# Kernel optimization log

Measured on AMD Instinct MI355X. Metric: run time of the kernel, lower is better.

The kernel has to match this reference:

```python
import jax, jax.numpy as jnp
import numpy as np

B, T, C = 4, 2048, 1024
H = 16
D = C // H  # head_dim = 64


def setup_inputs() -> dict:
    key = jax.random.key(0)
    ks = jax.random.split(key, 9)
    s = 1.0 / np.sqrt(C)
    return {
        "x": jax.random.normal(ks[0], (B, T, C), dtype=jnp.float32),
        "Wk": jax.random.uniform(ks[1], (C, C), jnp.float32, -s, s),
        "bk": jax.random.uniform(ks[2], (C,), jnp.float32, -s, s),
        "Wq": jax.random.uniform(ks[3], (C, C), jnp.float32, -s, s),
        "bq": jax.random.uniform(ks[4], (C,), jnp.float32, -s, s),
        "Wv": jax.random.uniform(ks[5], (C, C), jnp.float32, -s, s),
        "bv": jax.random.uniform(ks[6], (C,), jnp.float32, -s, s),
        "Wp": jax.random.uniform(ks[7], (C, C), jnp.float32, -s, s),
        "bp": jax.random.uniform(ks[8], (C,), jnp.float32, -s, s),
    }


def reference(x, Wk, bk, Wq, bq, Wv, bv, Wp, bp):
    # projections -> (B, H, T, D)
    def split_heads(y):
        return y.reshape(B, T, H, D).transpose(0, 2, 1, 3)

    k = split_heads(x @ Wk.T + bk)
    q = split_heads(x @ Wq.T + bq)
    v = split_heads(x @ Wv.T + bv)

    att = jnp.einsum("bhtd,bhsd->bhts", q, k) / np.sqrt(D).astype(np.float32)
    causal = jnp.tril(jnp.ones((T, T), dtype=bool))
    att = jnp.where(causal, att, -jnp.inf)
    att = jax.nn.softmax(att, axis=-1)

    y = jnp.einsum("bhts,bhsd->bhtd", att, v)  # (B,H,T,D)
    y = y.transpose(0, 2, 1, 3).reshape(B, T, C)
    return y @ Wp.T + bp
```

## Files before the change

### kernel.cpp

```cpp
#include <hip/hip_runtime.h>
#include <hip/hip_bf16.h>

typedef unsigned short u16;
typedef unsigned int u32;
typedef short short8 __attribute__((ext_vector_type(8)));
typedef short short4v __attribute__((ext_vector_type(4)));
typedef float f32x4 __attribute__((ext_vector_type(4)));
typedef unsigned int u32x4 __attribute__((ext_vector_type(4)));

#define MFMA16(a, b, c) __builtin_amdgcn_mfma_f32_16x16x32_bf16((a), (b), (c), 0, 0, 0)

constexpr int kB = 4, kT = 2048, kC = 1024, kH = 16, kD = 64;
constexpr int kBT = kB * kT;
constexpr long kQKV = (long)kB * kH * kT * kD;
constexpr float kSC = 0.125f * 1.4426950408889634f;

__device__ inline u16 f2bf(float f) {
    __hip_bfloat16 h = __float2bfloat16(f);
    return *reinterpret_cast<u16*>(&h);
}
__device__ inline u32 pkbf_trunc(float lo, float hi) {
    return __builtin_amdgcn_perm(__builtin_bit_cast(u32, hi),
                                 __builtin_bit_cast(u32, lo), 0x07060302u);
}
__device__ inline u32 pkbf_rne(float lo, float hi) {
    return ((u32)f2bf(hi) << 16) | (u32)f2bf(lo);
}

__device__ inline void cp16(const u16* g, u16* l) {
    __builtin_amdgcn_global_load_lds(
        (const __attribute__((address_space(1))) unsigned int*)g,
        (__attribute__((address_space(3))) unsigned int*)l, 16, 0, 0);
}

__global__ __launch_bounds__(256) void cast_kernel(
    const float* __restrict__ x,  const float* __restrict__ Wk,
    const float* __restrict__ Wq, const float* __restrict__ Wv,
    const float* __restrict__ Wp,
    u16* __restrict__ xb, u16* __restrict__ wkb, u16* __restrict__ wqb,
    u16* __restrict__ wvb, u16* __restrict__ wpb)
{
    const long id = (long)blockIdx.x * 256 + threadIdx.x;
    const float* src;
    u16* dst;
    long off;
    if (id < 2097152) {
        src = x; dst = xb; off = id;
    } else {
        const long w = (id - 2097152) >> 18;
        off = (id - 2097152) & 262143;
        src = (w == 0) ? Wk : (w == 1) ? Wq : (w == 2) ? Wv : Wp;
        dst = (w == 0) ? wkb : (w == 1) ? wqb : (w == 2) ? wvb : wpb;
    }
    f32x4 v = *(const f32x4*)&src[off * 4];
    short4v s = {(short)f2bf(v[0]), (short)f2bf(v[1]),
                 (short)f2bf(v[2]), (short)f2bf(v[3])};
    *(short4v*)&dst[off * 4] = s;
}


__global__ __launch_bounds__(256, 2) void qkv_gemm_bf16(
    const u16* __restrict__ xb, const u16* __restrict__ wall,
    const float* __restrict__ bk, const float* __restrict__ bq,
    const float* __restrict__ bv,
    u16* __restrict__ kw, u16* __restrict__ qw, u16* __restrict__ vw)
{
    __shared__ __align__(16) u16 A2[2][128 * 64];
    __shared__ __align__(16) u16 B2[2][128 * 64];

    const int tid = threadIdx.x;
    const int lane = tid & 63;
    const int wid = tid >> 6;
    const int l15 = lane & 15;
    const int quad = lane >> 4;
    const int wr = wid & 1;
    const int wc = wid >> 1;
    const int m0 = blockIdx.x * 128;
    const int n0c = blockIdx.y * 128;

    f32x4 zero = {0.f, 0.f, 0.f, 0.f};
    f32x4 acc[4][4];
#pragma unroll
    for (int i = 0; i < 4; ++i)
#pragma unroll
        for (int j = 0; j < 4; ++j) acc[i][j] = zero;

    const u16* aMaS[2]; const u16* aMbS[2];
    const u16* bNaS[2]; const u16* bNbS[2];
    int aMaD[2], aMbD[2], bNaD[2], bNbD[2];
#pragma unroll
    for (int q = 0; q < 2; ++q) {
        const int slot = q * 256 + tid;
        const int v = slot >> 3, ch = slot & 7;
        const int ra = ((v >> 5) << 6) + (v & 31);
        const int rb = ra + 32;
        aMaS[q] = xb + (long)(m0 + ra) * kC + ((ch ^ (ra & 7)) * 8);
        aMbS[q] = xb + (long)(m0 + rb) * kC + ((ch ^ (rb & 7)) * 8);
        aMaD[q] = ra * 64 + ch * 8;
        aMbD[q] = rb * 64 + ch * 8;
        bNaS[q] = wall + (long)(n0c + ra) * kC + ((ch ^ (ra & 7)) * 8);
        bNbS[q] = wall + (long)(n0c + rb) * kC + ((ch ^ (rb & 7)) * 8);
        bNaD[q] = ra * 64 + ch * 8;
        bNbD[q] = rb * 64 + ch * 8;
    }

    int aOff[4][2], bOff[4][2];
#pragma unroll
    for (int i = 0; i < 4; ++i) {
        const int row = wr * 64 + i * 16 + l15;
#pragma unroll
        for (int k2 = 0; k2 < 2; ++k2)
            aOff[i][k2] = row * 64 + (((k2 * 4 + quad) ^ (row & 7)) * 8);
    }
#pragma unroll
    for (int j = 0; j < 4; ++j) {
        const int row = wc * 64 + j * 16 + l15;
#pragma unroll
        for (int k2 = 0; k2 < 2; ++k2)
            bOff[j][k2] = row * 64 + (((k2 * 4 + quad) ^ (row & 7)) * 8);
    }

    cp16(bNaS[0], &B2[0][bNaD[0]]);
    cp16(bNaS[1], &B2[0][bNaD[1]]);
    cp16(aMaS[0], &A2[0][aMaD[0]]);
    cp16(aMaS[1], &A2[0][aMaD[1]]);
    cp16(aMbS[0], &A2[0][aMbD[0]]);
    cp16(aMbS[1], &A2[0][aMbD[1]]);
    cp16(bNbS[0], &B2[0][bNbD[0]]);
    cp16(bNbS[1], &B2[0][bNbD[1]]);

#pragma unroll 2
    for (int t = 0; t < 16; ++t) {
        const int c = t & 1;
        const u16* Ab = A2[c];
        const u16* Bb = B2[c];
        u16* An = A2[c ^ 1];
        u16* Bn = B2[c ^ 1];
        const long ko = (long)(t + 1) * 64;
        const bool pf = (t < 15);

        short8 amL[2][2], amH[2][2], bnL[2][2], bnH[2][2];

        asm volatile("s_waitcnt vmcnt(2)" ::: "memory");
        __builtin_amdgcn_s_barrier();
        __builtin_amdgcn_sched_barrier(0);
#pragma unroll
        for (int i = 0; i < 2; ++i)
#pragma unroll
            for (int k2 = 0; k2 < 2; ++k2)
                amL[i][k2] = *(const short8*)&Ab[aOff[i][k2]];
#pragma unroll
        for (int j = 0; j < 2; ++j)
#pragma unroll
            for (int k2 = 0; k2 < 2; ++k2)
                bnL[j][k2] = *(const short8*)&Bb[bOff[j][k2]];
        if (pf) {
            cp16(bNaS[0] + ko, &Bn[bNaD[0]]);
            cp16(bNaS[1] + ko, &Bn[bNaD[1]]);
        }
        asm volatile("s_waitcnt lgkmcnt(0)" ::: "memory");
        __builtin_amdgcn_sched_barrier(0);
        __builtin_amdgcn_s_setprio(1);
#pragma unroll
        for (int i = 0; i < 2; ++i)
#pragma unroll
            for (int j = 0; j < 2; ++j) {
                acc[i][j] = MFMA16(amL[i][0], bnL[j][0], acc[i][j]);
                acc[i][j] = MFMA16(amL[i][1], bnL[j][1], acc[i][j]);
            }
        __builtin_amdgcn_s_setprio(0);

#pragma unroll
        for (int i = 0; i < 2; ++i)
#pragma unroll
            for (int k2 = 0; k2 < 2; ++k2)
                amH[i][k2] = *(const short8*)&Ab[aOff[2 + i][k2]];
        if (pf) {
            cp16(aMaS[0] + ko, &An[aMaD[0]]);
            cp16(aMaS[1] + ko, &An[aMaD[1]]);
            cp16(aMbS[0] + ko, &An[aMbD[0]]);
            cp16(aMbS[1] + ko, &An[aMbD[1]]);
        }
        asm volatile("s_waitcnt lgkmcnt(0)" ::: "memory");
        __builtin_amdgcn_sched_barrier(0);
        __builtin_amdgcn_s_setprio(1);
#pragma unroll
        for (int i = 0; i < 2; ++i)
#pragma unroll
            for (int j = 0; j < 2; ++j) {
                acc[2 + i][j] = MFMA16(amH[i][0], bnL[j][0], acc[2 + i][j]);
                acc[2 + i][j] = MFMA16(amH[i][1], bnL[j][1], acc[2 + i][j]);
            }
        __builtin_amdgcn_s_setprio(0);

        if (pf) {
            asm volatile("s_waitcnt vmcnt(6)" ::: "memory");
        } else {
            asm volatile("s_waitcnt vmcnt(0)" ::: "memory");
        }
        __builtin_amdgcn_s_barrier();
        __builtin_amdgcn_sched_barrier(0);
#pragma unroll
        for (int j = 0; j < 2; ++j)
#pragma unroll
            for (int k2 = 0; k2 < 2; ++k2)
                bnH[j][k2] = *(const short8*)&Bb[bOff[2 + j][k2]];
        if (pf) {
            cp16(bNbS[0] + ko, &Bn[bNbD[0]]);
            cp16(bNbS[1] + ko, &Bn[bNbD[1]]);
        }
        asm volatile("s_waitcnt lgkmcnt(0)" ::: "memory");
        __builtin_amdgcn_sched_barrier(0);
        __builtin_amdgcn_s_setprio(1);
#pragma unroll
        for (int i = 0; i < 2; ++i)
#pragma unroll
            for (int j = 0; j < 2; ++j) {
                acc[i][2 + j] = MFMA16(amL[i][0], bnH[j][0], acc[i][2 + j]);
                acc[i][2 + j] = MFMA16(amL[i][1], bnH[j][1], acc[i][2 + j]);
            }
        __builtin_amdgcn_s_setprio(0);

        __builtin_amdgcn_s_setprio(1);
#pragma unroll
        for (int i = 0; i < 2; ++i)
#pragma unroll
            for (int j = 0; j < 2; ++j) {
                acc[2 + i][2 + j] = MFMA16(amH[i][0], bnH[j][0], acc[2 + i][2 + j]);
                acc[2 + i][2 + j] = MFMA16(amH[i][1], bnH[j][1], acc[2 + i][2 + j]);
            }
        __builtin_amdgcn_s_setprio(0);
    }

    const int z = (n0c >> 10);
    const float scale = (z == 1) ? kSC : 1.0f;
    const float* bias = (z == 0) ? bk : (z == 1) ? bq : bv;
#pragma unroll
    for (int j = 0; j < 4; ++j) {
        const int n = n0c + wc * 64 + j * 16 + l15;
        const int np = n & 1023;
        const float bias_f = bias[np];
        const int h = np >> 6, d = np & 63;
#pragma unroll
        for (int i = 0; i < 4; ++i) {
#pragma unroll
            for (int r = 0; r < 4; ++r) {
                const int m = m0 + wr * 64 + i * 16 + quad * 4 + r;
                const int b = m >> 11, tt = m & 2047;
                const float v = (acc[i][j][r] + bias_f) * scale;
                const int bh = b * kH + h;
                if (z == 2) {
                    vw[((long)bh * kD + d) * kT + tt] = f2bf(v);
                } else {
                    u16* dst = (z == 0) ? kw : qw;
                    dst[((long)bh * kT + tt) * kD + d] = f2bf(v);
                }
            }
        }
    }
}

__global__ __launch_bounds__(256) void qkv_gemm_kernel(
    const float* __restrict__ x,
    const float* __restrict__ Wk, const float* __restrict__ bk,
    const float* __restrict__ Wq, const float* __restrict__ bq,
    const float* __restrict__ Wv, const float* __restrict__ bv,
    u16* __restrict__ kw, u16* __restrict__ qw, u16* __restrict__ vw)
{
    __shared__ u16 As[128 * 32];
    __shared__ u16 Bs[128 * 32];
    const int tid = threadIdx.x;
    const int lane = tid & 63;
    const int wid = tid >> 6;
    const int l15 = lane & 15;
    const int quad = lane >> 4;
    const int m0 = blockIdx.x * 128;
    const int n0 = blockIdx.y * 128;
    const int z = blockIdx.z;

    const float* W = (z == 0) ? Wk : (z == 1) ? Wq : Wv;
    const float* bias = (z == 0) ? bk : (z == 1) ? bq : bv;

    f32x4 zero = {0.f, 0.f, 0.f, 0.f};
    f32x4 acc[4][4];
#pragma unroll
    for (int i = 0; i < 4; ++i)
#pragma unroll
        for (int j = 0; j < 4; ++j) acc[i][j] = zero;

    const int wm = (wid & 1) * 64;
    const int wn = (wid >> 1) * 64;
    const int row4 = tid >> 3;
    const int col4 = (tid & 7) * 4;

    for (int k0 = 0; k0 < kC; k0 += 32) {
#pragma unroll
        for (int p = 0; p < 4; ++p) {
            const int r = p * 32 + row4;
            f32x4 xa = *(const f32x4*)&x[(long)(m0 + r) * kC + k0 + col4];
            f32x4 wa = *(const f32x4*)&W[(long)(n0 + r) * kC + k0 + col4];
            short4v xs = {(short)f2bf(xa[0]), (short)f2bf(xa[1]),
                          (short)f2bf(xa[2]), (short)f2bf(xa[3])};
            short4v wsv = {(short)f2bf(wa[0]), (short)f2bf(wa[1]),
                           (short)f2bf(wa[2]), (short)f2bf(wa[3])};
            *(short4v*)&As[r * 32 + col4] = xs;
            *(short4v*)&Bs[r * 32 + col4] = wsv;
        }
        __syncthreads();
        short8 af[4], bfr[4];
#pragma unroll
        for (int mt = 0; mt < 4; ++mt)
            af[mt] = *(const short8*)&As[(wm + mt * 16 + l15) * 32 + quad * 8];
#pragma unroll
        for (int nt = 0; nt < 4; ++nt)
            bfr[nt] = *(const short8*)&Bs[(wn + nt * 16 + l15) * 32 + quad * 8];
#pragma unroll
        for (int mt = 0; mt < 4; ++mt)
#pragma unroll
            for (int nt = 0; nt < 4; ++nt)
                acc[mt][nt] = MFMA16(af[mt], bfr[nt], acc[mt][nt]);
        __syncthreads();
    }

    const float scale = (z == 1) ? kSC : 1.0f;
#pragma unroll
    for (int nt = 0; nt < 4; ++nt) {
        const int n = n0 + wn + nt * 16 + l15;
        const float bias_f = bias[n];
        const int h = n >> 6, d = n & 63;
#pragma unroll
        for (int mt = 0; mt < 4; ++mt) {
#pragma unroll
            for (int r = 0; r < 4; ++r) {
                const int m = m0 + wm + mt * 16 + quad * 4 + r;
                const int b = m >> 11, t = m & 2047;
                const float v = (acc[mt][nt][r] + bias_f) * scale;
                const int bh = b * kH + h;
                if (z == 2) {
                    vw[((long)bh * kD + d) * kT + t] = f2bf(v);
                } else {
                    u16* dst = (z == 0) ? kw : qw;
                    dst[((long)bh * kT + t) * kD + d] = f2bf(v);
                }
            }
        }
    }
}

__global__ __launch_bounds__(256, 4) void attn_kernel(
    const u16* qw, const u16* kw, const u16* vw, u16* ow)
{
    __shared__ u16 Ks[2][64 * 64];
    __shared__ u16 VT[2][64 * 64];

    const int tid = threadIdx.x;
    const int lane = tid & 63;
    const int wid = tid >> 6;
    const int l15 = lane & 15;
    const int quad = lane >> 4;
    const int id = blockIdx.x;
    const int bh = id & 63;
    constexpr int pperm[16] = {15, 14, 13, 12, 0, 1, 2, 3,
                               11, 10, 9, 8, 4, 5, 6, 7};
    const int p = pperm[id >> 6];
    const int p2 = 2 * p;
    const int n_st = p2 + 2;
    const int tw = p * 128 + wid * 32;

    const float NEG = -1.0e30f;
    f32x4 zero = {0.f, 0.f, 0.f, 0.f};
    const short8 onesf = {(short)0x3F80, (short)0x3F80, (short)0x3F80, (short)0x3F80,
                          (short)0x3F80, (short)0x3F80, (short)0x3F80, (short)0x3F80};

    const int rl7 = l15 & 7;

    const u16* kbase = kw + (long)bh * kT * kD;
    const u16* vbase = vw + (long)bh * kD * kT;

    const u16* kp[2];
    const u16* vp[2];
    int sdst[2];
#pragma unroll
    for (int q = 0; q < 2; ++q) {
        const int slot = q * 256 + tid;
        const int row = slot >> 3;
        const int c = slot & 7;
        const int off = (c ^ (row & 7)) * 8;
        kp[q] = kbase + (long)row * kD + off;
        vp[q] = vbase + (long)row * kT + off;
        sdst[q] = slot * 8;
    }

    auto stage = [&](int buf, int st) {
        u16* kd = Ks[buf];
        u16* vd = VT[buf];
#pragma unroll
        for (int q = 0; q < 2; ++q) {
            cp16(kp[q] + (long)st * (64 * kD), kd + sdst[q]);
            cp16(vp[q] + st * 64,              vd + sdst[q]);
        }
    };

    short8 qf[2][2];
#pragma unroll
    for (int g = 0; g < 2; ++g) {
        const u16* qp = qw + ((long)bh * kT + tw + g * 16 + l15) * kD;
        qf[g][0] = *(const short8*)&qp[quad * 8];
        qf[g][1] = *(const short8*)&qp[32 + quad * 8];
    }

    stage(0, 0);
    stage(1, 1);
    __syncthreads();

    f32x4 oacc[4][2];
#pragma unroll
    for (int mo = 0; mo < 4; ++mo)
#pragma unroll
        for (int g = 0; g < 2; ++g) oacc[mo][g] = zero;
    f32x4 lsum[2] = {zero, zero};

    for (int st = 0; st < n_st; ++st) {
        const int cur = st & 1;
        const u16* K_ = Ks[cur];
        const u16* V_ = VT[cur];

        f32x4 sacc[4][2];
        __builtin_amdgcn_s_setprio(1);
#pragma unroll
        for (int ms = 0; ms < 4; ++ms) {
            const int row = ms * 16 + l15;
            short8 kf0 = *(const short8*)&K_[row * 64 + ((quad ^ rl7) * 8)];
            short8 kf1 = *(const short8*)&K_[row * 64 + (((4 + quad) ^ rl7) * 8)];
#pragma unroll
            for (int g = 0; g < 2; ++g) {
                sacc[ms][g] = MFMA16(kf0, qf[g][0], zero);
                sacc[ms][g] = MFMA16(kf1, qf[g][1], sacc[ms][g]);
            }
        }
        __builtin_amdgcn_s_setprio(0);

        const int dg = st - p2;
        if (dg >= 0) {
#pragma unroll
            for (int g = 0; g < 2; ++g) {
                const int off = wid * 32 + g * 16 + l15 - dg * 64;
#pragma unroll
                for (int ms = 0; ms < 4; ++ms)
#pragma unroll
                    for (int r = 0; r < 4; ++r)
                        if (ms * 16 + quad * 4 + r > off) sacc[ms][g][r] = NEG;
            }
        }

        short8 pfr[2][2];
#pragma unroll
        for (int g = 0; g < 2; ++g) {
#pragma unroll
            for (int k2 = 0; k2 < 2; ++k2) {
                const int msA = k2 * 2, msB = k2 * 2 + 1;
                const float a0 = exp2f(sacc[msA][g][0]);
                const float a1 = exp2f(sacc[msA][g][1]);
                const float a2 = exp2f(sacc[msA][g][2]);
                const float a3 = exp2f(sacc[msA][g][3]);
                const float b0 = exp2f(sacc[msB][g][0]);
                const float b1 = exp2f(sacc[msB][g][1]);
                const float b2 = exp2f(sacc[msB][g][2]);
                const float b3 = exp2f(sacc[msB][g][3]);
                const u32 LA = pkbf_trunc(a0, a1), HA = pkbf_trunc(a2, a3);
                const u32 LB = pkbf_trunc(b0, b1), HB = pkbf_trunc(b2, b3);
                auto pL = __builtin_amdgcn_permlane32_swap(LA, LB, false, false);
                auto pH = __builtin_amdgcn_permlane32_swap(HA, HB, false, false);
                auto rL = __builtin_amdgcn_permlane16_swap(pL[0], pL[1], false, false);
                auto rH = __builtin_amdgcn_permlane16_swap(pH[0], pH[1], false, false);
                u32x4 w;
                w[0] = rL[0]; w[1] = rH[0]; w[2] = rL[1]; w[3] = rH[1];
                pfr[g][k2] = __builtin_bit_cast(short8, w);
            }
        }

#pragma unroll
        for (int g = 0; g < 2; ++g) {
            lsum[g] = MFMA16(onesf, pfr[g][0], lsum[g]);
            lsum[g] = MFMA16(onesf, pfr[g][1], lsum[g]);
        }

        __builtin_amdgcn_s_setprio(1);
#pragma unroll
        for (int mo = 0; mo < 4; ++mo) {
            const int row = mo * 16 + l15;
            short8 vf0 = *(const short8*)&V_[row * 64 + ((quad ^ rl7) * 8)];
            short8 vf1 = *(const short8*)&V_[row * 64 + (((4 + quad) ^ rl7) * 8)];
#pragma unroll
            for (int g = 0; g < 2; ++g) {
                oacc[mo][g] = MFMA16(vf0, pfr[g][0], oacc[mo][g]);
                oacc[mo][g] = MFMA16(vf1, pfr[g][1], oacc[mo][g]);
            }
        }
        __builtin_amdgcn_s_setprio(0);

        if (st + 1 < n_st) {
            __syncthreads();
            if (st + 2 < n_st) stage(cur, st + 2);
        }
    }

#pragma unroll
    for (int g = 0; g < 2; ++g) {
        const float inv = 1.0f / lsum[g][0];
        const int t = tw + g * 16 + l15;
        u16* op = ow + ((long)bh * kT + t) * kD;
#pragma unroll
        for (int mo = 0; mo < 4; ++mo) {
            uint2 ov;
            ov.x = pkbf_rne(oacc[mo][g][0] * inv, oacc[mo][g][1] * inv);
            ov.y = pkbf_rne(oacc[mo][g][2] * inv, oacc[mo][g][3] * inv);
            *(uint2*)&op[mo * 16 + quad * 4] = ov;
        }
    }
}

__global__ __launch_bounds__(256, 2) void out_gemm_bf16(
    const u16* __restrict__ ob, const u16* __restrict__ wpb,
    const float* __restrict__ bp, float* __restrict__ out)
{
    __shared__ __align__(16) u16 A2[2][128 * 64];
    __shared__ __align__(16) u16 B2[2][128 * 64];

    const int tid = threadIdx.x;
    const int lane = tid & 63;
    const int wid = tid >> 6;
    const int l15 = lane & 15;
    const int quad = lane >> 4;
    const int wr = wid & 1;
    const int wc = wid >> 1;
    const int m0 = blockIdx.x * 128;
    const int n0 = blockIdx.y * 128;

    f32x4 zero = {0.f, 0.f, 0.f, 0.f};
    f32x4 acc[4][4];
#pragma unroll
    for (int i = 0; i < 4; ++i)
#pragma unroll
        for (int j = 0; j < 4; ++j) acc[i][j] = zero;

    const u16* aMaS[2]; const u16* aMbS[2];
    const u16* bNaS[2]; const u16* bNbS[2];
    int aMaD[2], aMbD[2], bNaD[2], bNbD[2];
#pragma unroll
    for (int q = 0; q < 2; ++q) {
        const int slot = q * 256 + tid;
        const int v = slot >> 3, ch = slot & 7;
        const int ra = ((v >> 5) << 6) + (v & 31);
        const int rb = ra + 32;
        const int mA = m0 + ra, mB = m0 + rb;
        aMaS[q] = ob + (((long)(mA >> 11) * kH) * kT + (mA & 2047)) * kD
                  + ((ch ^ (ra & 7)) * 8);
        aMbS[q] = ob + (((long)(mB >> 11) * kH) * kT + (mB & 2047)) * kD
                  + ((ch ^ (rb & 7)) * 8);
        aMaD[q] = ra * 64 + ch * 8;
        aMbD[q] = rb * 64 + ch * 8;
        bNaS[q] = wpb + (long)(n0 + ra) * kC + ((ch ^ (ra & 7)) * 8);
        bNbS[q] = wpb + (long)(n0 + rb) * kC + ((ch ^ (rb & 7)) * 8);
        bNaD[q] = ra * 64 + ch * 8;
        bNbD[q] = rb * 64 + ch * 8;
    }

    int aOff[4][2], bOff[4][2];
#pragma unroll
    for (int i = 0; i < 4; ++i) {
        const int row = wr * 64 + i * 16 + l15;
#pragma unroll
        for (int k2 = 0; k2 < 2; ++k2)
            aOff[i][k2] = row * 64 + (((k2 * 4 + quad) ^ (row & 7)) * 8);
    }
#pragma unroll
    for (int j = 0; j < 4; ++j) {
        const int row = wc * 64 + j * 16 + l15;
#pragma unroll
        for (int k2 = 0; k2 < 2; ++k2)
            bOff[j][k2] = row * 64 + (((k2 * 4 + quad) ^ (row & 7)) * 8);
    }

    cp16(bNaS[0], &B2[0][bNaD[0]]);
    cp16(bNaS[1], &B2[0][bNaD[1]]);
    cp16(aMaS[0], &A2[0][aMaD[0]]);
    cp16(aMaS[1], &A2[0][aMaD[1]]);
    cp16(aMbS[0], &A2[0][aMbD[0]]);
    cp16(aMbS[1], &A2[0][aMbD[1]]);
    cp16(bNbS[0], &B2[0][bNbD[0]]);
    cp16(bNbS[1], &B2[0][bNbD[1]]);

#pragma unroll 2
    for (int t = 0; t < 16; ++t) {
        const int c = t & 1;
        const u16* Ab = A2[c];
        const u16* Bb = B2[c];
        u16* An = A2[c ^ 1];
        u16* Bn = B2[c ^ 1];
        const long koA = (long)(t + 1) * kT * kD;
        const long koB = (long)(t + 1) * 64;
        const bool pf = (t < 15);

        short8 amL[2][2], amH[2][2], bnL[2][2], bnH[2][2];

        asm volatile("s_waitcnt vmcnt(2)" ::: "memory");
        __builtin_amdgcn_s_barrier();
        __builtin_amdgcn_sched_barrier(0);
#pragma unroll
        for (int i = 0; i < 2; ++i)
#pragma unroll
            for (int k2 = 0; k2 < 2; ++k2)
                amL[i][k2] = *(const short8*)&Ab[aOff[i][k2]];
#pragma unroll
        for (int j = 0; j < 2; ++j)
#pragma unroll
            for (int k2 = 0; k2 < 2; ++k2)
                bnL[j][k2] = *(const short8*)&Bb[bOff[j][k2]];
        if (pf) {
            cp16(bNaS[0] + koB, &Bn[bNaD[0]]);
            cp16(bNaS[1] + koB, &Bn[bNaD[1]]);
        }
        asm volatile("s_waitcnt lgkmcnt(0)" ::: "memory");
        __builtin_amdgcn_sched_barrier(0);
        __builtin_amdgcn_s_setprio(1);
#pragma unroll
        for (int i = 0; i < 2; ++i)
#pragma unroll
            for (int j = 0; j < 2; ++j) {
                acc[i][j] = MFMA16(amL[i][0], bnL[j][0], acc[i][j]);
                acc[i][j] = MFMA16(amL[i][1], bnL[j][1], acc[i][j]);
            }
        __builtin_amdgcn_s_setprio(0);

#pragma unroll
        for (int i = 0; i < 2; ++i)
#pragma unroll
            for (int k2 = 0; k2 < 2; ++k2)
                amH[i][k2] = *(const short8*)&Ab[aOff[2 + i][k2]];
        if (pf) {
            cp16(aMaS[0] + koA, &An[aMaD[0]]);
            cp16(aMaS[1] + koA, &An[aMaD[1]]);
            cp16(aMbS[0] + koA, &An[aMbD[0]]);
            cp16(aMbS[1] + koA, &An[aMbD[1]]);
        }
        asm volatile("s_waitcnt lgkmcnt(0)" ::: "memory");
        __builtin_amdgcn_sched_barrier(0);
        __builtin_amdgcn_s_setprio(1);
#pragma unroll
        for (int i = 0; i < 2; ++i)
#pragma unroll
            for (int j = 0; j < 2; ++j) {
                acc[2 + i][j] = MFMA16(amH[i][0], bnL[j][0], acc[2 + i][j]);
                acc[2 + i][j] = MFMA16(amH[i][1], bnL[j][1], acc[2 + i][j]);
            }
        __builtin_amdgcn_s_setprio(0);

        if (pf) {
            asm volatile("s_waitcnt vmcnt(6)" ::: "memory");
        } else {
            asm volatile("s_waitcnt vmcnt(0)" ::: "memory");
        }
        __builtin_amdgcn_s_barrier();
        __builtin_amdgcn_sched_barrier(0);
#pragma unroll
        for (int j = 0; j < 2; ++j)
#pragma unroll
            for (int k2 = 0; k2 < 2; ++k2)
                bnH[j][k2] = *(const short8*)&Bb[bOff[2 + j][k2]];
        if (pf) {
            cp16(bNbS[0] + koB, &Bn[bNbD[0]]);
            cp16(bNbS[1] + koB, &Bn[bNbD[1]]);
        }
        asm volatile("s_waitcnt lgkmcnt(0)" ::: "memory");
        __builtin_amdgcn_sched_barrier(0);
        __builtin_amdgcn_s_setprio(1);
#pragma unroll
        for (int i = 0; i < 2; ++i)
#pragma unroll
            for (int j = 0; j < 2; ++j) {
                acc[i][2 + j] = MFMA16(amL[i][0], bnH[j][0], acc[i][2 + j]);
                acc[i][2 + j] = MFMA16(amL[i][1], bnH[j][1], acc[i][2 + j]);
            }
        __builtin_amdgcn_s_setprio(0);

        __builtin_amdgcn_s_setprio(1);
#pragma unroll
        for (int i = 0; i < 2; ++i)
#pragma unroll
            for (int j = 0; j < 2; ++j) {
                acc[2 + i][2 + j] = MFMA16(amH[i][0], bnH[j][0], acc[2 + i][2 + j]);
                acc[2 + i][2 + j] = MFMA16(amH[i][1], bnH[j][1], acc[2 + i][2 + j]);
            }
        __builtin_amdgcn_s_setprio(0);
    }

#pragma unroll
    for (int j = 0; j < 4; ++j) {
        const int n = n0 + wc * 64 + j * 16 + l15;
        const float bias_f = bp[n];
#pragma unroll
        for (int i = 0; i < 4; ++i) {
#pragma unroll
            for (int r = 0; r < 4; ++r) {
                const int m = m0 + wr * 64 + i * 16 + quad * 4 + r;
                out[(long)m * kC + n] = acc[i][j][r] + bias_f;
            }
        }
    }
}

__global__ __launch_bounds__(256) void out_gemm_kernel(
    const u16* __restrict__ ow, const float* __restrict__ Wp,
    const float* __restrict__ bp, float* __restrict__ out)
{
    __shared__ u16 As[128 * 32];
    __shared__ u16 Bs[128 * 32];
    const int tid = threadIdx.x;
    const int lane = tid & 63;
    const int wid = tid >> 6;
    const int l15 = lane & 15;
    const int quad = lane >> 4;
    const int m0 = blockIdx.x * 128;
    const int n0 = blockIdx.y * 128;

    f32x4 zero = {0.f, 0.f, 0.f, 0.f};
    f32x4 acc[4][4];
#pragma unroll
    for (int i = 0; i < 4; ++i)
#pragma unroll
        for (int j = 0; j < 4; ++j) acc[i][j] = zero;

    const int wm = (wid & 1) * 64;
    const int wn = (wid >> 1) * 64;

    const int r0 = tid >> 2;
    const int kkA = (tid & 3) * 8;
    const int r1 = r0 + 64;
    const int row4 = tid >> 3;
    const int col4 = (tid & 7) * 4;

    for (int k0 = 0; k0 < kC; k0 += 32) {
        {
            const int m = m0 + r0, b = m >> 11, t = m & 2047;
            const int kk = k0 + kkA, h = kk >> 6, d = kk & 63;
            *(short8*)&As[r0 * 32 + kkA] =
                *(const short8*)&ow[(((long)b * kH + h) * kT + t) * kD + d];
        }
        {
            const int m = m0 + r1, b = m >> 11, t = m & 2047;
            const int kk = k0 + kkA, h = kk >> 6, d = kk & 63;
            *(short8*)&As[r1 * 32 + kkA] =
                *(const short8*)&ow[(((long)b * kH + h) * kT + t) * kD + d];
        }
#pragma unroll
        for (int p = 0; p < 4; ++p) {
            const int r = p * 32 + row4;
            f32x4 wa = *(const f32x4*)&Wp[(long)(n0 + r) * kC + k0 + col4];
            short4v wsv = {(short)f2bf(wa[0]), (short)f2bf(wa[1]),
                           (short)f2bf(wa[2]), (short)f2bf(wa[3])};
            *(short4v*)&Bs[r * 32 + col4] = wsv;
        }
        __syncthreads();
        short8 af[4], bfr[4];
#pragma unroll
        for (int mt = 0; mt < 4; ++mt)
            af[mt] = *(const short8*)&As[(wm + mt * 16 + l15) * 32 + quad * 8];
#pragma unroll
        for (int nt = 0; nt < 4; ++nt)
            bfr[nt] = *(const short8*)&Bs[(wn + nt * 16 + l15) * 32 + quad * 8];
#pragma unroll
        for (int mt = 0; mt < 4; ++mt)
#pragma unroll
            for (int nt = 0; nt < 4; ++nt)
                acc[mt][nt] = MFMA16(af[mt], bfr[nt], acc[mt][nt]);
        __syncthreads();
    }

#pragma unroll
    for (int nt = 0; nt < 4; ++nt) {
        const int n = n0 + wn + nt * 16 + l15;
        const float bias_f = bp[n];
#pragma unroll
        for (int mt = 0; mt < 4; ++mt) {
#pragma unroll
            for (int r = 0; r < 4; ++r) {
                const int m = m0 + wm + mt * 16 + quad * 4 + r;
                out[(long)m * kC + n] = acc[mt][nt][r] + bias_f;
            }
        }
    }
}

extern "C" void kernel_launch(void* const* d_in, const int* in_sizes, int n_in,
                              void* d_out, int out_size, void* d_ws, size_t ws_size,
                              hipStream_t stream) {
    const float* x  = (const float*)d_in[0];
    const float* Wk = (const float*)d_in[1];
    const float* bk = (const float*)d_in[2];
    const float* Wq = (const float*)d_in[3];
    const float* bq = (const float*)d_in[4];
    const float* Wv = (const float*)d_in[5];
    const float* bv = (const float*)d_in[6];
    const float* Wp = (const float*)d_in[7];
    const float* bp = (const float*)d_in[8];
    float* out = (float*)d_out;

    u16* ws = (u16*)d_ws;
    const size_t kNeed = 72ull * 1024 * 1024;

    if (ws_size >= kNeed) {
        u16* k_ws = ws;
        u16* q_ws = ws + kQKV;
        u16* v_ws = ws + 2 * kQKV;
        u16* xb   = ws + 3 * kQKV;
        u16* o_ws = xb;
        u16* wkb  = ws + 4 * kQKV;
        u16* wqb  = wkb + (long)kC * kC;
        u16* wvb  = wqb + (long)kC * kC;
        u16* wpb  = wvb + (long)kC * kC;

        cast_kernel<<<12288, 256, 0, stream>>>(x, Wk, Wq, Wv, Wp,
                                               xb, wkb, wqb, wvb, wpb);
        qkv_gemm_bf16<<<dim3(kBT / 128, 24), 256, 0, stream>>>(
            xb, wkb, bk, bq, bv, k_ws, q_ws, v_ws);
        attn_kernel<<<1024, 256, 0, stream>>>(q_ws, k_ws, v_ws, o_ws);
        out_gemm_bf16<<<dim3(kBT / 128, kC / 128), 256, 0, stream>>>(
            o_ws, wpb, bp, out);
    } else {
        u16* k_ws = ws;
        u16* q_ws = ws + kQKV;
        u16* v_ws = ws + 2 * kQKV;
        u16* o_ws = q_ws;

        qkv_gemm_kernel<<<dim3(kBT / 128, kC / 128, 3), 256, 0, stream>>>(
            x, Wk, bk, Wq, bq, Wv, bv, k_ws, q_ws, v_ws);
        attn_kernel<<<1024, 256, 0, stream>>>(q_ws, k_ws, v_ws, o_ws);
        out_gemm_kernel<<<dim3(kBT / 128, kC / 128), 256, 0, stream>>>(
            o_ws, Wp, bp, out);
    }
}
```

Measured before the change: 260.5 us.

## Use 512-thread blocks with simplified double-buffered pipeline in bf16 GEMMs

Both bf16 GEMM kernels (QKV and output projection) move from 4 waves per 128x128 tile to 8 waves, with each wave computing a 64x32 sub-tile. The hand-interleaved split-phase pipeline, with its explicit vmcnt waits and staggered prefetches, is replaced by a plain double buffer: stage two k-tiles up front, then __syncthreads and prefetch k-tile t+2 each iteration. The aim is more waves to hide latency and simpler code. In exchange, launch bounds of (512,4) put heavy pressure on registers, which can cause spills. LDS of 64KB per block limits how many blocks actually co-reside, and much of the fine-grained overlap of loads with MFMA work is lost.

```diff
diff --git a/kernel.cpp b/kernel.cpp
--- a/kernel.cpp
+++ b/kernel.cpp
@@ -59,7 +59,7 @@
 }
 
 
-__global__ __launch_bounds__(256, 2) void qkv_gemm_bf16(
+__global__ __launch_bounds__(512, 4) void qkv_gemm_bf16(
     const u16* __restrict__ xb, const u16* __restrict__ wall,
     const float* __restrict__ bk, const float* __restrict__ bq,
     const float* __restrict__ bv,
@@ -79,32 +79,33 @@
     const int n0c = blockIdx.y * 128;
 
     f32x4 zero = {0.f, 0.f, 0.f, 0.f};
-    f32x4 acc[4][4];
+    f32x4 acc[4][2];
 #pragma unroll
     for (int i = 0; i < 4; ++i)
 #pragma unroll
-        for (int j = 0; j < 4; ++j) acc[i][j] = zero;
-
-    const u16* aMaS[2]; const u16* aMbS[2];
-    const u16* bNaS[2]; const u16* bNbS[2];
-    int aMaD[2], aMbD[2], bNaD[2], bNbD[2];
+        for (int j = 0; j < 2; ++j) acc[i][j] = zero;
+
+    const u16* aS[2]; const u16* bS[2];
+    int sD[2];
 #pragma unroll
     for (int q = 0; q < 2; ++q) {
-        const int slot = q * 256 + tid;
-        const int v = slot >> 3, ch = slot & 7;
-        const int ra = ((v >> 5) << 6) + (v & 31);
-        const int rb = ra + 32;
-        aMaS[q] = xb + (long)(m0 + ra) * kC + ((ch ^ (ra & 7)) * 8);
-        aMbS[q] = xb + (long)(m0 + rb) * kC + ((ch ^ (rb & 7)) * 8);
-        aMaD[q] = ra * 64 + ch * 8;
-        aMbD[q] = rb * 64 + ch * 8;
-        bNaS[q] = wall + (long)(n0c + ra) * kC + ((ch ^ (ra & 7)) * 8);
-        bNbS[q] = wall + (long)(n0c + rb) * kC + ((ch ^ (rb & 7)) * 8);
-        bNaD[q] = ra * 64 + ch * 8;
-        bNbD[q] = rb * 64 + ch * 8;
-    }
-
-    int aOff[4][2], bOff[4][2];
+        const int slot = q * 512 + tid;
+        const int row = slot >> 3, ch = slot & 7;
+        aS[q] = xb + (long)(m0 + row) * kC + ((ch ^ (row & 7)) * 8);
+        bS[q] = wall + (long)(n0c + row) * kC + ((ch ^ (row & 7)) * 8);
+        sD[q] = row * 64 + ch * 8;
+    }
+
+    auto stage = [&](int buf, int t) {
+        const long ko = (long)t * 64;
+#pragma unroll
+        for (int q = 0; q < 2; ++q) {
+            cp16(aS[q] + ko, &A2[buf][sD[q]]);
+            cp16(bS[q] + ko, &B2[buf][sD[q]]);
+        }
+    };
+
+    int aOff[4][2], bOff[2][2];
 #pragma unroll
     for (int i = 0; i < 4; ++i) {
         const int row = wr * 64 + i * 16 + l15;
@@ -113,131 +114,56 @@
             aOff[i][k2] = row * 64 + (((k2 * 4 + quad) ^ (row & 7)) * 8);
     }
 #pragma unroll
-    for (int j = 0; j < 4; ++j) {
-        const int row = wc * 64 + j * 16 + l15;
+    for (int j = 0; j < 2; ++j) {
+        const int row = wc * 32 + j * 16 + l15;
 #pragma unroll
         for (int k2 = 0; k2 < 2; ++k2)
             bOff[j][k2] = row * 64 + (((k2 * 4 + quad) ^ (row & 7)) * 8);
     }
 
-    cp16(bNaS[0], &B2[0][bNaD[0]]);
-    cp16(bNaS[1], &B2[0][bNaD[1]]);
-    cp16(aMaS[0], &A2[0][aMaD[0]]);
-    cp16(aMaS[1], &A2[0][aMaD[1]]);
-    cp16(aMbS[0], &A2[0][aMbD[0]]);
-    cp16(aMbS[1], &A2[0][aMbD[1]]);
-    cp16(bNbS[0], &B2[0][bNbD[0]]);
-    cp16(bNbS[1], &B2[0][bNbD[1]]);
-
-#pragma unroll 2
+    stage(0, 0);
+    stage(1, 1);
+    __syncthreads();
+
     for (int t = 0; t < 16; ++t) {
         const int c = t & 1;
         const u16* Ab = A2[c];
         const u16* Bb = B2[c];
-        u16* An = A2[c ^ 1];
-        u16* Bn = B2[c ^ 1];
-        const long ko = (long)(t + 1) * 64;
-        const bool pf = (t < 15);
-
-        short8 amL[2][2], amH[2][2], bnL[2][2], bnH[2][2];
-
-        asm volatile("s_waitcnt vmcnt(2)" ::: "memory");
-        __builtin_amdgcn_s_barrier();
-        __builtin_amdgcn_sched_barrier(0);
-#pragma unroll
-        for (int i = 0; i < 2; ++i)
+
+        short8 am[4][2], bn[2][2];
+#pragma unroll
+        for (int i = 0; i < 4; ++i)
 #pragma unroll
             for (int k2 = 0; k2 < 2; ++k2)
-                amL[i][k2] = *(const short8*)&Ab[aOff[i][k2]];
+                am[i][k2] = *(const short8*)&Ab[aOff[i][k2]];
 #pragma unroll
         for (int j = 0; j < 2; ++j)
 #pragma unroll
             for (int k2 = 0; k2 < 2; ++k2)
-                bnL[j][k2] = *(const short8*)&Bb[bOff[j][k2]];
-        if (pf) {
-            cp16(bNaS[0] + ko, &Bn[bNaD[0]]);
-            cp16(bNaS[1] + ko, &Bn[bNaD[1]]);
-        }
-        asm volatile("s_waitcnt lgkmcnt(0)" ::: "memory");
-        __builtin_amdgcn_sched_barrier(0);
+                bn[j][k2] = *(const short8*)&Bb[bOff[j][k2]];
+
         __builtin_amdgcn_s_setprio(1);
 #pragma unroll
-        for (int i = 0; i < 2; ++i)
+        for (int i = 0; i < 4; ++i)
 #pragma unroll
             for (int j = 0; j < 2; ++j) {
-                acc[i][j] = MFMA16(amL[i][0], bnL[j][0], acc[i][j]);
-                acc[i][j] = MFMA16(amL[i][1], bnL[j][1], acc[i][j]);
+                acc[i][j] = MFMA16(am[i][0], bn[j][0], acc[i][j]);
+                acc[i][j] = MFMA16(am[i][1], bn[j][1], acc[i][j]);
             }
         __builtin_amdgcn_s_setprio(0);
 
-#pragma unroll
-        for (int i = 0; i < 2; ++i)
-#pragma unroll
-            for (int k2 = 0; k2 < 2; ++k2)
-                amH[i][k2] = *(const short8*)&Ab[aOff[2 + i][k2]];
-        if (pf) {
-            cp16(aMaS[0] + ko, &An[aMaD[0]]);
-            cp16(aMaS[1] + ko, &An[aMaD[1]]);
-            cp16(aMbS[0] + ko, &An[aMbD[0]]);
-            cp16(aMbS[1] + ko, &An[aMbD[1]]);
-        }
-        asm volatile("s_waitcnt lgkmcnt(0)" ::: "memory");
-        __builtin_amdgcn_sched_barrier(0);
-        __builtin_amdgcn_s_setprio(1);
-#pragma unroll
-        for (int i = 0; i < 2; ++i)
-#pragma unroll
-            for (int j = 0; j < 2; ++j) {
-                acc[2 + i][j] = MFMA16(amH[i][0], bnL[j][0], acc[2 + i][j]);
-                acc[2 + i][j] = MFMA16(amH[i][1], bnL[j][1], acc[2 + i][j]);
-            }
-        __builtin_amdgcn_s_setprio(0);
-
-        if (pf) {
-            asm volatile("s_waitcnt vmcnt(6)" ::: "memory");
-        } else {
-            asm volatile("s_waitcnt vmcnt(0)" ::: "memory");
-        }
-        __builtin_amdgcn_s_barrier();
-        __builtin_amdgcn_sched_barrier(0);
-#pragma unroll
-        for (int j = 0; j < 2; ++j)
-#pragma unroll
-            for (int k2 = 0; k2 < 2; ++k2)
-                bnH[j][k2] = *(const short8*)&Bb[bOff[2 + j][k2]];
-        if (pf) {
-            cp16(bNbS[0] + ko, &Bn[bNbD[0]]);
-            cp16(bNbS[1] + ko, &Bn[bNbD[1]]);
-        }
-        asm volatile("s_waitcnt lgkmcnt(0)" ::: "memory");
-        __builtin_amdgcn_sched_barrier(0);
-        __builtin_amdgcn_s_setprio(1);
-#pragma unroll
-        for (int i = 0; i < 2; ++i)
-#pragma unroll
-            for (int j = 0; j < 2; ++j) {
-                acc[i][2 + j] = MFMA16(amL[i][0], bnH[j][0], acc[i][2 + j]);
-                acc[i][2 + j] = MFMA16(amL[i][1], bnH[j][1], acc[i][2 + j]);
-            }
-        __builtin_amdgcn_s_setprio(0);
-
-        __builtin_amdgcn_s_setprio(1);
-#pragma unroll
-        for (int i = 0; i < 2; ++i)
-#pragma unroll
-            for (int j = 0; j < 2; ++j) {
-                acc[2 + i][2 + j] = MFMA16(amH[i][0], bnH[j][0], acc[2 + i][2 + j]);
-                acc[2 + i][2 + j] = MFMA16(amH[i][1], bnH[j][1], acc[2 + i][2 + j]);
-            }
-        __builtin_amdgcn_s_setprio(0);
+        if (t + 1 < 16) {
+            __syncthreads();
+            if (t + 2 < 16) stage(c, t + 2);
+        }
     }
 
     const int z = (n0c >> 10);
     const float scale = (z == 1) ? kSC : 1.0f;
     const float* bias = (z == 0) ? bk : (z == 1) ? bq : bv;
 #pragma unroll
-    for (int j = 0; j < 4; ++j) {
-        const int n = n0c + wc * 64 + j * 16 + l15;
+    for (int j = 0; j < 2; ++j) {
+        const int n = n0c + wc * 32 + j * 16 + l15;
         const int np = n & 1023;
         const float bias_f = bias[np];
         const int h = np >> 6, d = np & 63;
@@ -520,7 +446,7 @@
     }
 }
 
-__global__ __launch_bounds__(256, 2) void out_gemm_bf16(
+__global__ __launch_bounds__(512, 4) void out_gemm_bf16(
     const u16* __restrict__ ob, const u16* __restrict__ wpb,
     const float* __restrict__ bp, float* __restrict__ out)
 {
@@ -538,35 +464,35 @@
     const int n0 = blockIdx.y * 128;
 
     f32x4 zero = {0.f, 0.f, 0.f, 0.f};
-    f32x4 acc[4][4];
+    f32x4 acc[4][2];
 #pragma unroll
     for (int i = 0; i < 4; ++i)
 #pragma unroll
-        for (int j = 0; j < 4; ++j) acc[i][j] = zero;
-
-    const u16* aMaS[2]; const u16* aMbS[2];
-    const u16* bNaS[2]; const u16* bNbS[2];
-    int aMaD[2], aMbD[2], bNaD[2], bNbD[2];
+        for (int j = 0; j < 2; ++j) acc[i][j] = zero;
+
+    const u16* aS[2]; const u16* bS[2];
+    int sD[2];
 #pragma unroll
     for (int q = 0; q < 2; ++q) {
-        const int slot = q * 256 + tid;
-        const int v = slot >> 3, ch = slot & 7;
-        const int ra = ((v >> 5) << 6) + (v & 31);
-        const int rb = ra + 32;
-        const int mA = m0 + ra, mB = m0 + rb;
-        aMaS[q] = ob + (((long)(mA >> 11) * kH) * kT + (mA & 2047)) * kD
-                  + ((ch ^ (ra & 7)) * 8);
-        aMbS[q] = ob + (((long)(mB >> 11) * kH) * kT + (mB & 2047)) * kD
-                  + ((ch ^ (rb & 7)) * 8);
-        aMaD[q] = ra * 64 + ch * 8;
-        aMbD[q] = rb * 64 + ch * 8;
-        bNaS[q] = wpb + (long)(n0 + ra) * kC + ((ch ^ (ra & 7)) * 8);
-        bNbS[q] = wpb + (long)(n0 + rb) * kC + ((ch ^ (rb & 7)) * 8);
-        bNaD[q] = ra * 64 + ch * 8;
-        bNbD[q] = rb * 64 + ch * 8;
-    }
-
-    int aOff[4][2], bOff[4][2];
+        const int slot = q * 512 + tid;
+        const int row = slot >> 3, ch = slot & 7;
+        const int m = m0 + row, b = m >> 11, trow = m & 2047;
+        aS[q] = ob + (((long)b * kH) * kT + trow) * kD + ((ch ^ (row & 7)) * 8);
+        bS[q] = wpb + (long)(n0 + row) * kC + ((ch ^ (row & 7)) * 8);
+        sD[q] = row * 64 + ch * 8;
+    }
+
+    auto stage = [&](int buf, int t) {
+        const long koA = (long)t * kT * kD;
+        const long koB = (long)t * 64;
+#pragma unroll
+        for (int q = 0; q < 2; ++q) {
+            cp16(aS[q] + koA, &A2[buf][sD[q]]);
+            cp16(bS[q] + koB, &B2[buf][sD[q]]);
+        }
+    };
+
+    int aOff[4][2], bOff[2][2];
 #pragma unroll
     for (int i = 0; i < 4; ++i) {
         const int row = wr * 64 + i * 16 + l15;
@@ -575,129 +501,53 @@
             aOff[i][k2] = row * 64 + (((k2 * 4 + quad) ^ (row & 7)) * 8);
     }
 #pragma unroll
-    for (int j = 0; j < 4; ++j) {
-        const int row = wc * 64 + j * 16 + l15;
+    for (int j = 0; j < 2; ++j) {
+        const int row = wc * 32 + j * 16 + l15;
 #pragma unroll
         for (int k2 = 0; k2 < 2; ++k2)
             bOff[j][k2] = row * 64 + (((k2 * 4 + quad) ^ (row & 7)) * 8);
     }
 
-    cp16(bNaS[0], &B2[0][bNaD[0]]);
-    cp16(bNaS[1], &B2[0][bNaD[1]]);
-    cp16(aMaS[0], &A2[0][aMaD[0]]);
-    cp16(aMaS[1], &A2[0][aMaD[1]]);
-    cp16(aMbS[0], &A2[0][aMbD[0]]);
-    cp16(aMbS[1], &A2[0][aMbD[1]]);
-    cp16(bNbS[0], &B2[0][bNbD[0]]);
-    cp16(bNbS[1], &B2[0][bNbD[1]]);
-
-#pragma unroll 2
+    stage(0, 0);
+    stage(1, 1);
+    __syncthreads();
+
     for (int t = 0; t < 16; ++t) {
         const int c = t & 1;
         const u16* Ab = A2[c];
         const u16* Bb = B2[c];
-        u16* An = A2[c ^ 1];
-        u16* Bn = B2[c ^ 1];
-        const long koA = (long)(t + 1) * kT * kD;
-        const long koB = (long)(t + 1) * 64;
-        const bool pf = (t < 15);
-
-        short8 amL[2][2], amH[2][2], bnL[2][2], bnH[2][2];
-
-        asm volatile("s_waitcnt vmcnt(2)" ::: "memory");
-        __builtin_amdgcn_s_barrier();
-        __builtin_amdgcn_sched_barrier(0);
-#pragma unroll
-        for (int i = 0; i < 2; ++i)
+
+        short8 am[4][2], bn[2][2];
+#pragma unroll
+        for (int i = 0; i < 4; ++i)
 #pragma unroll
             for (int k2 = 0; k2 < 2; ++k2)
-                amL[i][k2] = *(const short8*)&Ab[aOff[i][k2]];
+                am[i][k2] = *(const short8*)&Ab[aOff[i][k2]];
 #pragma unroll
         for (int j = 0; j < 2; ++j)
 #pragma unroll
             for (int k2 = 0; k2 < 2; ++k2)
-                bnL[j][k2] = *(const short8*)&Bb[bOff[j][k2]];
-        if (pf) {
-            cp16(bNaS[0] + koB, &Bn[bNaD[0]]);
-            cp16(bNaS[1] + koB, &Bn[bNaD[1]]);
-        }
-        asm volatile("s_waitcnt lgkmcnt(0)" ::: "memory");
-        __builtin_amdgcn_sched_barrier(0);
+                bn[j][k2] = *(const short8*)&Bb[bOff[j][k2]];
+
         __builtin_amdgcn_s_setprio(1);
 #pragma unroll
-        for (int i = 0; i < 2; ++i)
+        for (int i = 0; i < 4; ++i)
 #pragma unroll
             for (int j = 0; j < 2; ++j) {
-                acc[i][j] = MFMA16(amL[i][0], bnL[j][0], acc[i][j]);
-                acc[i][j] = MFMA16(amL[i][1], bnL[j][1], acc[i][j]);
+                acc[i][j] = MFMA16(am[i][0], bn[j][0], acc[i][j]);
+                acc[i][j] = MFMA16(am[i][1], bn[j][1], acc[i][j]);
             }
         __builtin_amdgcn_s_setprio(0);
 
-#pragma unroll
-        for (int i = 0; i < 2; ++i)
-#pragma unroll
-            for (int k2 = 0; k2 < 2; ++k2)
-                amH[i][k2] = *(const short8*)&Ab[aOff[2 + i][k2]];
-        if (pf) {
-            cp16(aMaS[0] + koA, &An[aMaD[0]]);
-            cp16(aMaS[1] + koA, &An[aMaD[1]]);
-            cp16(aMbS[0] + koA, &An[aMbD[0]]);
-            cp16(aMbS[1] + koA, &An[aMbD[1]]);
-        }
-        asm volatile("s_waitcnt lgkmcnt(0)" ::: "memory");
-        __builtin_amdgcn_sched_barrier(0);
-        __builtin_amdgcn_s_setprio(1);
-#pragma unroll
-        for (int i = 0; i < 2; ++i)
-#pragma unroll
-            for (int j = 0; j < 2; ++j) {
-                acc[2 + i][j] = MFMA16(amH[i][0], bnL[j][0], acc[2 + i][j]);
-                acc[2 + i][j] = MFMA16(amH[i][1], bnL[j][1], acc[2 + i][j]);
-            }
-        __builtin_amdgcn_s_setprio(0);
-
-        if (pf) {
-            asm volatile("s_waitcnt vmcnt(6)" ::: "memory");
-        } else {
-            asm volatile("s_waitcnt vmcnt(0)" ::: "memory");
-        }
-        __builtin_amdgcn_s_barrier();
-        __builtin_amdgcn_sched_barrier(0);
-#pragma unroll
-        for (int j = 0; j < 2; ++j)
-#pragma unroll
-            for (int k2 = 0; k2 < 2; ++k2)
-                bnH[j][k2] = *(const short8*)&Bb[bOff[2 + j][k2]];
-        if (pf) {
-            cp16(bNbS[0] + koB, &Bn[bNbD[0]]);
-            cp16(bNbS[1] + koB, &Bn[bNbD[1]]);
-        }
-        asm volatile("s_waitcnt lgkmcnt(0)" ::: "memory");
-        __builtin_amdgcn_sched_barrier(0);
-        __builtin_amdgcn_s_setprio(1);
-#pragma unroll
-        for (int i = 0; i < 2; ++i)
-#pragma unroll
-            for (int j = 0; j < 2; ++j) {
-                acc[i][2 + j] = MFMA16(amL[i][0], bnH[j][0], acc[i][2 + j]);
-                acc[i][2 + j] = MFMA16(amL[i][1], bnH[j][1], acc[i][2 + j]);
-            }
-        __builtin_amdgcn_s_setprio(0);
-
-        __builtin_amdgcn_s_setprio(1);
-#pragma unroll
-        for (int i = 0; i < 2; ++i)
-#pragma unroll
-            for (int j = 0; j < 2; ++j) {
-                acc[2 + i][2 + j] = MFMA16(amH[i][0], bnH[j][0], acc[2 + i][2 + j]);
-                acc[2 + i][2 + j] = MFMA16(amH[i][1], bnH[j][1], acc[2 + i][2 + j]);
-            }
-        __builtin_amdgcn_s_setprio(0);
-    }
-
-#pragma unroll
-    for (int j = 0; j < 4; ++j) {
-        const int n = n0 + wc * 64 + j * 16 + l15;
+        if (t + 1 < 16) {
+            __syncthreads();
+            if (t + 2 < 16) stage(c, t + 2);
+        }
+    }
+
+#pragma unroll
+    for (int j = 0; j < 2; ++j) {
+        const int n = n0 + wc * 32 + j * 16 + l15;
         const float bias_f = bp[n];
 #pragma unroll
         for (int i = 0; i < 4; ++i) {
@@ -822,10 +672,10 @@
 
         cast_kernel<<<12288, 256, 0, stream>>>(x, Wk, Wq, Wv, Wp,
                                                xb, wkb, wqb, wvb, wpb);
-        qkv_gemm_bf16<<<dim3(kBT / 128, 24), 256, 0, stream>>>(
+        qkv_gemm_bf16<<<dim3(kBT / 128, 24), 512, 0, stream>>>(
             xb, wkb, bk, bq, bv, k_ws, q_ws, v_ws);
         attn_kernel<<<1024, 256, 0, stream>>>(q_ws, k_ws, v_ws, o_ws);
-        out_gemm_bf16<<<dim3(kBT / 128, kC / 128), 256, 0, stream>>>(
+        out_gemm_bf16<<<dim3(kBT / 128, kC / 128), 512, 0, stream>>>(
             o_ws, wpb, bp, out);
     } else {
         u16* k_ws = ws;
```

After: 246.9 us. 1.05x faster.
